# Kernel tuning notes

Measured on AMD Instinct MI355X. Metric: run time of the kernel, lower is better.

Reference implementation:

```python
import jax, jax.numpy as jnp
import numpy as np

NUM_CLASSES = 15
ANGLE_BINS = 90
ANGLE_SCALE = float(np.pi / 2 / ANGLE_BINS)
TOPK, A_ALPHA, A_BETA = 13, 1.0, 6.0
F_ALPHA, F_GAMMA = 0.75, 2.0
W_CLS, W_BOX, W_ANGLE = 1.0, 2.5, 0.05
EPS = 1e-9


def make_anchors(img=1024, strides=(8, 16, 32)):
    pts, strs = [], []
    for s in strides:
        n = img // s
        xs = (np.arange(n, dtype=np.float32) + 0.5) * s  # pixel-space centers
        X, Y = np.meshgrid(xs, xs)
        pts.append(np.stack([X.ravel(), Y.ravel()], -1))
        strs.append(np.full((n * n, 1), s, np.float32))
    return np.concatenate(pts)[None].astype(np.float32), np.concatenate(strs)[None]


def decode_boxes(anchor_points, reg_dist, raw_angles, stride_tensor, angle_proj):
    # DFL-style angle: softmax over bins projected onto angle values
    angle = jnp.einsum('bna,a->bn', jax.nn.softmax(raw_angles, axis=-1), angle_proj)  # [B,N]
    lt, rb = reg_dist[..., :2], reg_dist[..., 2:]
    off = (rb - lt) * 0.5
    c, s = jnp.cos(angle), jnp.sin(angle)
    ox = off[..., 0] * c - off[..., 1] * s
    oy = off[..., 0] * s + off[..., 1] * c
    xy = jnp.stack([ox, oy], -1) * stride_tensor + anchor_points
    wh = (lt + rb) * stride_tensor
    return jnp.concatenate([xy, wh, angle[..., None]], -1)  # [B,N,5]


def _cov(b):
    # rotated box -> 2D Gaussian covariance terms
    w, h, a = b[..., 2], b[..., 3], b[..., 4]
    A, B = w * w / 12.0, h * h / 12.0
    c, s = jnp.cos(a), jnp.sin(a)
    return A * c * c + B * s * s, A * s * s + B * c * c, (A - B) * c * s


def probiou_hd(b1, b2, eps=1e-3):
    # Hellinger distance between Gaussian boxes; probiou similarity = 1 - hd
    x1, y1, x2, y2 = b1[..., 0], b1[..., 1], b2[..., 0], b2[..., 1]
    a1, bb1, c1 = _cov(b1)
    a2, bb2, c2 = _cov(b2)
    denom = (a1 + a2) * (bb1 + bb2) - (c1 + c2) ** 2 + eps
    t1 = ((a1 + a2) * (y1 - y2) ** 2 + (bb1 + bb2) * (x1 - x2) ** 2) / denom * 0.25
    t2 = ((c1 + c2) * (x2 - x1) * (y1 - y2)) / denom * 0.5
    det1 = jnp.maximum(a1 * bb1 - c1 * c1, 0.0)
    det2 = jnp.maximum(a2 * bb2 - c2 * c2, 0.0)
    t3 = 0.5 * jnp.log(denom / (4.0 * jnp.sqrt(det1 * det2) + eps) + eps)
    bd = jnp.clip(t1 + t2 + t3, eps, 100.0)
    return jnp.sqrt(1.0 - jnp.exp(-bd) + 1e-7)


def assign(pred_scores, pred_boxes, anchor_points, gt_labels, gt_boxes, pad_gt_mask, bg_index):
    B, M = gt_labels.shape[:2]
    N = pred_boxes.shape[1]
    C = pred_scores.shape[-1]
    lbl = gt_labels[..., 0]  # [B,M]
    # rotated ProbIoU between every GT and every pred box: [B,M,N]
    ious = jnp.maximum(1.0 - probiou_hd(gt_boxes[:, :, None, :], pred_boxes[:, None, :, :]), 0.0)
    # gather pred class score at each gt's label: [B,M,N]
    scores = jnp.einsum('bnc,bmc->bmn', pred_scores, jax.nn.one_hot(lbl, C, dtype=pred_scores.dtype))
    align = (scores ** A_ALPHA) * (ious ** A_BETA)
    # anchor-center inside rotated GT box
    dx = anchor_points[:, None, :, 0] - gt_boxes[:, :, None, 0]
    dy = anchor_points[:, None, :, 1] - gt_boxes[:, :, None, 1]
    ca, sa = jnp.cos(gt_boxes[:, :, None, 4]), jnp.sin(gt_boxes[:, :, None, 4])
    xr = dx * ca + dy * sa
    yr = -dx * sa + dy * ca
    in_gt = (jnp.abs(xr) < gt_boxes[:, :, None, 2] * 0.5) & (jnp.abs(yr) < gt_boxes[:, :, None, 3] * 0.5)
    mask_cand = in_gt.astype(align.dtype) * pad_gt_mask  # [B,M,N]
    # top-k alignment candidates per GT
    topv, topi = jax.lax.top_k(align * mask_cand, TOPK)
    valid = (topv > EPS).astype(align.dtype)
    bi = jnp.arange(B)[:, None, None]
    mi = jnp.arange(M)[None, :, None]
    topk_mask = jnp.zeros((B, M, N), align.dtype).at[bi, mi, topi].max(valid)
    mask_pos = topk_mask * mask_cand
    # resolve anchors matched to multiple GTs via max IoU
    fg = mask_pos.sum(1)  # [B,N]
    is_max_iou = jax.nn.one_hot(jnp.argmax(ious, axis=1), M, axis=1, dtype=align.dtype)
    mask_pos = jnp.where(fg[:, None, :] > 1, is_max_iou, mask_pos)
    fg = mask_pos.sum(1)
    tgt_idx = jnp.argmax(mask_pos, axis=1)  # [B,N]
    fg_mask = fg > 0
    assigned_labels = jnp.where(fg_mask, jnp.take_along_axis(lbl, tgt_idx, axis=1), bg_index)
    assigned_boxes = jnp.take_along_axis(gt_boxes, tgt_idx[..., None], axis=1)  # [B,N,5]
    # normalize alignment metric by per-GT max IoU / max align
    align_pos = align * mask_pos
    max_align = align_pos.max(-1, keepdims=True)
    max_iou = (ious * mask_pos).max(-1, keepdims=True)
    norm_align = (align_pos * max_iou / (max_align + EPS)).max(1)  # [B,N]
    onehot = jax.nn.one_hot(assigned_labels, C + 1, dtype=align.dtype)[..., :C]
    assigned_scores = onehot * norm_align[..., None]
    return assigned_labels, assigned_boxes, assigned_scores


def _bce_logits(x, t):
    return jnp.maximum(x, 0.0) - x * t + jnp.log1p(jnp.exp(-jnp.abs(x)))


def compute_loss(cls_logits, reg_dist, raw_angles, gt_labels, gt_boxes, valid_mask,
                 anchor_points, stride_tensor, angle_proj):
    C = NUM_CLASSES
    decoded = decode_boxes(anchor_points, reg_dist, raw_angles, stride_tensor, angle_proj)
    cls_scores = jax.nn.sigmoid(cls_logits)
    al, ab, ascore = assign(jax.lax.stop_gradient(cls_scores), jax.lax.stop_gradient(decoded),
                            anchor_points, gt_labels, gt_boxes, valid_mask, C)
    score_sum = jnp.maximum(ascore.sum(), 1.0)
    # varifocal classification loss
    onehot = jax.nn.one_hot(al, C + 1, dtype=cls_logits.dtype)[..., :C]
    fw = F_ALPHA * (cls_scores ** F_GAMMA) * (1.0 - onehot) + ascore * onehot
    loss_cls = (_bce_logits(cls_logits, ascore) * fw).sum() / score_sum
    # ProbIoU box loss over positives, weighted by assigned scores
    posf = (al != C).astype(cls_logits.dtype)
    iou_loss = probiou_hd(decoded, ab)  # [B,N]
    bw = ascore.sum(-1)
    loss_box = (iou_loss * bw * posf).sum() / score_sum
    # DFL angle loss: interpolate CE between neighboring bins
    t = jnp.clip(ab[..., 4] / ANGLE_SCALE, 0.0, ANGLE_BINS - 0.01)
    li = t.astype(jnp.int32)
    ri = jnp.minimum(li + 1, ANGLE_BINS)
    lw = ri.astype(t.dtype) - t
    rw = 1.0 - lw
    logp = jax.nn.log_softmax(raw_angles, axis=-1)
    ce_l = -jnp.take_along_axis(logp, li[..., None], axis=-1)[..., 0]
    ce_r = -jnp.take_along_axis(logp, ri[..., None], axis=-1)[..., 0]
    npos = jnp.maximum(posf.sum(), 1.0)
    loss_angle = ((ce_l * lw + ce_r * rw) * posf).sum() / npos
    total = W_CLS * loss_cls + W_BOX * loss_box + W_ANGLE * loss_angle
    return total, loss_cls, loss_box, loss_angle


def setup_inputs() -> dict:
    key = jax.random.key(0)
    ks = jax.random.split(key, 8)
    B, M, C, AB = 16, 64, NUM_CLASSES, ANGLE_BINS
    anchor_np, stride_np = make_anchors()
    N = anchor_np.shape[1]  # 21504
    cls_logits = jax.random.normal(ks[0], (B, N, C), jnp.float32) - 2.0
    reg_dist = jax.random.uniform(ks[1], (B, N, 4), jnp.float32, 0.0, 6.0)
    raw_angles = jax.random.normal(ks[2], (B, N, AB + 1), jnp.float32)
    gt_labels = jax.random.randint(ks[3], (B, M, 1), 0, C)
    cxy = jax.random.uniform(ks[4], (B, M, 2), jnp.float32, 32.0, 992.0)
    wh = jax.random.uniform(ks[5], (B, M, 2), jnp.float32, 16.0, 160.0)
    ang = jax.random.uniform(ks[6], (B, M, 1), jnp.float32, 0.0, float(np.pi / 2) - 1e-3)
    gt_boxes = jnp.concatenate([cxy, wh, ang], -1)
    valid_mask = (jax.random.uniform(ks[7], (B, M, 1)) < 0.8).astype(jnp.float32)
    angle_proj = jnp.arange(AB + 1, dtype=jnp.float32) * ANGLE_SCALE
    return dict(cls_logits=cls_logits, reg_dist=reg_dist, raw_angles=raw_angles,
                gt_labels=gt_labels, gt_boxes=gt_boxes, valid_mask=valid_mask,
                anchor_points=jnp.asarray(anchor_np), stride_tensor=jnp.asarray(stride_np),
                angle_proj=angle_proj)


def reference(cls_logits, reg_dist, raw_angles, gt_labels, gt_boxes, valid_mask,
              anchor_points, stride_tensor, angle_proj):
    return compute_loss(cls_logits, reg_dist, raw_angles, gt_labels, gt_boxes, valid_mask,
                        anchor_points, stride_tensor, angle_proj)
```

## Files before the change

### kernel.cpp

```cpp
#include <hip/hip_runtime.h>

#define TK 13
#define EPSA 1e-9f
#define MMAX 128
#define CMAX 1024
#define DROWS 64
#define A1F 91

__device__ __forceinline__ float frcp(float x) { return __builtin_amdgcn_rcpf(x); }

__device__ __forceinline__ float hd_cov(float x1, float y1, float a1, float b1, float c1, float sd1,
                                        float x2, float y2, float a2, float b2, float c2, float sd2) {
    float sa = a1 + a2, sb = b1 + b2, sc = c1 + c2;
    float denom = sa * sb - sc * sc + 1e-3f;
    float inv = frcp(denom);
    float dy = y1 - y2, dx = x1 - x2;
    float t1 = (sa * dy * dy + sb * dx * dx) * inv * 0.25f;
    float t2 = sc * (x2 - x1) * (y1 - y2) * inv * 0.5f;
    float t3 = 0.5f * __logf(denom * frcp(4.0f * sd1 * sd2 + 1e-3f) + 1e-3f);
    float bd = fminf(fmaxf(t1 + t2 + t3, 1e-3f), 100.0f);
    return sqrtf(1.0f - __expf(-bd) + 1e-7f);
}

__device__ __forceinline__ void cov5(float w, float h, float ang,
                                     float& ca, float& cb, float& cc, float& sd) {
    float A = w * w * (1.0f / 12.0f), B = h * h * (1.0f / 12.0f);
    float c = __cosf(ang), s = __sinf(ang);
    ca = A * c * c + B * s * s;
    cb = A * s * s + B * c * c;
    cc = (A - B) * c * s;
    sd = sqrtf(fmaxf(ca * cb - cc * cc, 0.0f));
}

__global__ __launch_bounds__(256) void k_decode(
    const float* __restrict__ reg, const float* __restrict__ rawang,
    const float* __restrict__ anch, const float* __restrict__ strd,
    float* __restrict__ dec6, float* __restrict__ lse_out,
    int BN, int N) {
    __shared__ float srow[DROWS * A1F];
    int r0 = blockIdx.x * DROWS;
    if (r0 >= BN) return;
    int tid = threadIdx.x;
    const float* gsrc = rawang + (size_t)r0 * A1F;
    int lim = min(DROWS, BN - r0) * A1F;
    for (int k = tid; k < lim; k += 256) srow[k] = gsrc[k];
    __syncthreads();
    int row = tid >> 2, sub = tid & 3;
    int idx = r0 + row;
    if (idx >= BN) return;
    int j0 = sub * 23;
    int jn = (sub == 3) ? 22 : 23;
    const float* rp = srow + row * A1F + j0;
    float s = 0.0f, num = 0.0f;
#pragma unroll
    for (int i = 0; i < 23; ++i) {
        if (i < jn) {
            float e = __expf(rp[i]);
            s += e;
            num = fmaf(e, (float)(j0 + i), num);
        }
    }
    s += __shfl_xor(s, 1); num += __shfl_xor(num, 1);
    s += __shfl_xor(s, 2); num += __shfl_xor(num, 2);
    if (sub == 0) {
        float ang = 0.017453292519943295f * num * frcp(s);
        float lse = __logf(s);
        int n = idx % N;
        float4 rg = *(const float4*)(reg + (size_t)idx * 4);
        float l0 = rg.x, l1 = rg.y, rr0 = rg.z, rr1 = rg.w;
        float offx = (rr0 - l0) * 0.5f, offy = (rr1 - l1) * 0.5f;
        float c = __cosf(ang), sn = __sinf(ang);
        float ox = offx * c - offy * sn, oy = offx * sn + offy * c;
        float st = strd[n];
        float x = ox * st + anch[2 * n];
        float y = oy * st + anch[2 * n + 1];
        float w = (l0 + rr0) * st, hh = (l1 + rr1) * st;
        float ca, cb, cc, sd;
        cov5(w, hh, ang, ca, cb, cc, sd);
        float* d = dec6 + (size_t)idx * 6;
        d[0] = x; d[1] = y; d[2] = ca; d[3] = cb; d[4] = cc; d[5] = sd;
        lse_out[idx] = lse;
    }
}

__global__ __launch_bounds__(256) void k_topk(
    const float* __restrict__ dec6, const float* __restrict__ cls,
    const float* __restrict__ gtb, const int* __restrict__ gtl,
    const float* __restrict__ vmask,
    int* __restrict__ fg, int* __restrict__ tgtc,
    int B, int M, int N, int C) {
    int m = blockIdx.x, b = blockIdx.y;
    if (vmask[b * M + m] == 0.0f) return;
    const float* g = gtb + (size_t)(b * M + m) * 5;
    float gx = g[0], gy = g[1], gw = g[2], gh = g[3], gang = g[4];
    float gca, gcb, gcc, gsd;
    cov5(gw, gh, gang, gca, gcb, gcc, gsd);
    float cA = __cosf(gang), sA = __sinf(gang);
    int lbl = gtl[b * M + m];
    float hw = 0.5f * gw, hh2 = 0.5f * gh;
    float hx = fabsf(hw * cA) + fabsf(hh2 * sA);
    float hy = fabsf(hw * sA) + fabsf(hh2 * cA);
    int tid = threadIdx.x;
    size_t bN = (size_t)b * N;

    __shared__ int cnt;
    __shared__ float cval[CMAX];
    __shared__ int cidx[CMAX];
    if (tid == 0) cnt = 0;
    __syncthreads();

    const int off_[3] = {0, 16384, 20480};
    const int gs_[3]  = {128, 64, 32};
    const float st_[3] = {8.0f, 16.0f, 32.0f};
#pragma unroll
    for (int lv = 0; lv < 3; ++lv) {
        float st = st_[lv];
        int gs = gs_[lv], off = off_[lv];
        float ist = frcp(st);
        int i0 = (int)floorf((gx - hx) * ist - 0.5f);
        int i1 = (int)ceilf((gx + hx) * ist - 0.5f);
        int j0 = (int)floorf((gy - hy) * ist - 0.5f);
        int j1 = (int)ceilf((gy + hy) * ist - 0.5f);
        i0 = max(i0, 0); j0 = max(j0, 0);
        i1 = min(i1, gs - 1); j1 = min(j1, gs - 1);
        int w = i1 - i0 + 1, hgt = j1 - j0 + 1;
        int tot = (w > 0 && hgt > 0) ? w * hgt : 0;
        for (int t = tid; t < tot; t += 256) {
            int ii = i0 + t % w, jj = j0 + t / w;
            float ax = (ii + 0.5f) * st, ay = (jj + 0.5f) * st;
            float dx = ax - gx, dy = ay - gy;
            float xr = dx * cA + dy * sA;
            float yr = -dx * sA + dy * cA;
            if (fabsf(xr) < hw && fabsf(yr) < hh2) {
                int n = off + jj * gs + ii;
                const float* d = dec6 + (bN + n) * 6;
                float hd = hd_cov(gx, gy, gca, gcb, gcc, gsd,
                                  d[0], d[1], d[2], d[3], d[4], d[5]);
                float iou = fmaxf(1.0f - hd, 0.0f);
                float xl = cls[(bN + n) * C + lbl];
                float p = frcp(1.0f + __expf(-xl));
                float i2 = iou * iou;
                float v = p * (i2 * i2 * i2);
                if (v > EPSA) {
                    int pos = atomicAdd(&cnt, 1);
                    if (pos < CMAX) { cval[pos] = v; cidx[pos] = n; }
                }
            }
        }
    }
    __syncthreads();

    int total = min(cnt, CMAX);
    int rounds = min(total, TK);
    if (tid < 64) {
        for (int r = 0; r < rounds; ++r) {
            float bv = -1.0f; int bn = 0x7fffffff; int bp = -1;
            for (int j = tid; j < total; j += 64) {
                float v = cval[j];
                int nn = cidx[j];
                if (v > bv || (v == bv && nn < bn)) { bv = v; bn = nn; bp = j; }
            }
            for (int o = 32; o; o >>= 1) {
                float ov = __shfl_xor(bv, o);
                int on = __shfl_xor(bn, o);
                int op = __shfl_xor(bp, o);
                if (ov > bv || (ov == bv && on < bn)) { bv = ov; bn = on; bp = op; }
            }
            if (tid == 0) {
                atomicAdd(&fg[bN + bn], 1);
                atomicMax(&tgtc[bN + bn], m);
            }
            if ((bp & 63) == tid) cval[bp] = -2.0f;
        }
    }
}

__global__ __launch_bounds__(256) void k_select(
    const float* __restrict__ dec6, const float* __restrict__ cls,
    const float* __restrict__ gtb, const int* __restrict__ gtl,
    const int* __restrict__ fg, const int* __restrict__ tgtc,
    int* __restrict__ tgt_out, float* __restrict__ align_out,
    unsigned int* __restrict__ max_align, unsigned int* __restrict__ max_iou,
    int B, int M, int N, int C) {
    __shared__ float gx[MMAX], gy[MMAX], ga[MMAX], gb[MMAX], gc[MMAX], gsd[MMAX];
    __shared__ int glb[MMAX];
    int b = blockIdx.y;
    int tid = threadIdx.x;
    if (tid < M) {
        const float* g = gtb + (size_t)(b * M + tid) * 5;
        float ca, cb, cc, sd;
        cov5(g[2], g[3], g[4], ca, cb, cc, sd);
        gx[tid] = g[0]; gy[tid] = g[1]; ga[tid] = ca; gb[tid] = cb; gc[tid] = cc; gsd[tid] = sd;
        glb[tid] = gtl[b * M + tid];
    }
    __syncthreads();
    int n = blockIdx.x * 256 + tid;
    if (n >= N) return;
    size_t bN = (size_t)b * N;
    int f = fg[bN + n];
    if (f == 0) {
        tgt_out[bN + n] = -1;
        align_out[bN + n] = 0.0f;
        return;
    }
    const float* d = dec6 + (bN + n) * 6;
    float px = d[0], py = d[1], pa = d[2], pb = d[3], pc = d[4], psd = d[5];
    int mstar;
    float ioustar;
    if (f == 1) {
        mstar = tgtc[bN + n];
        float hd = hd_cov(gx[mstar], gy[mstar], ga[mstar], gb[mstar], gc[mstar], gsd[mstar],
                          px, py, pa, pb, pc, psd);
        ioustar = fmaxf(1.0f - hd, 0.0f);
    } else {
        float best = -1.0f; int bm = 0;
        for (int mm = 0; mm < M; mm++) {
            float hd = hd_cov(gx[mm], gy[mm], ga[mm], gb[mm], gc[mm], gsd[mm],
                              px, py, pa, pb, pc, psd);
            float iou = fmaxf(1.0f - hd, 0.0f);
            if (iou > best) { best = iou; bm = mm; }
        }
        mstar = bm; ioustar = best;
    }
    int lbl = glb[mstar];
    float xl = cls[(bN + n) * C + lbl];
    float p = frcp(1.0f + __expf(-xl));
    float i2 = ioustar * ioustar;
    float al = p * (i2 * i2 * i2);
    tgt_out[bN + n] = mstar;
    align_out[bN + n] = al;
    atomicMax(&max_align[b * M + mstar], __float_as_uint(al));
    atomicMax(&max_iou[b * M + mstar], __float_as_uint(ioustar));
}

__global__ __launch_bounds__(256) void k_loss(
    const float* __restrict__ dec6, const float* __restrict__ cls,
    const float* __restrict__ rawang, const float* __restrict__ lse_in,
    const float* __restrict__ gtb, const int* __restrict__ gtl,
    const int* __restrict__ tgt_in, const float* __restrict__ align_in,
    const float* __restrict__ max_align, const float* __restrict__ max_iou,
    float* __restrict__ pblk,
    int B, int M, int N, int C, int A1) {
    __shared__ float gx[MMAX], gy[MMAX], ga[MMAX], gb[MMAX], gc[MMAX], gsd[MMAX], gan[MMAX];
    __shared__ int glb[MMAX];
    int b = blockIdx.y;
    int tid = threadIdx.x;
    if (tid < M) {
        const float* g = gtb + (size_t)(b * M + tid) * 5;
        float ca, cb, cc, sd;
        cov5(g[2], g[3], g[4], ca, cb, cc, sd);
        gx[tid] = g[0]; gy[tid] = g[1]; ga[tid] = ca; gb[tid] = cb; gc[tid] = cc; gsd[tid] = sd;
        gan[tid] = g[4];
        glb[tid] = gtl[b * M + tid];
    }
    __syncthreads();
    int n = blockIdx.x * 256 + tid;
    float s_cls = 0.0f, s_box = 0.0f, s_ang = 0.0f, s_asc = 0.0f, s_pos = 0.0f;
    if (n < N) {
        size_t bN = (size_t)b * N;
        int tg = tgt_in[bN + n];
        int lbl = -1;
        float norm = 0.0f;
        if (tg >= 0) {
            lbl = glb[tg];
            norm = align_in[bN + n] * max_iou[b * M + tg] * frcp(max_align[b * M + tg] + 1e-9f);
            const float* d = dec6 + (bN + n) * 6;
            float hd = hd_cov(d[0], d[1], d[2], d[3], d[4], d[5],
                              gx[tg], gy[tg], ga[tg], gb[tg], gc[tg], gsd[tg]);
            s_box = hd * norm;
            s_asc = norm;
            s_pos = 1.0f;
            float tt = fminf(fmaxf(gan[tg] * 57.29577951308232f, 0.0f), 89.99f);
            int li = (int)tt;
            int ri = min(li + 1, 90);
            float lw = (float)ri - tt;
            float rw = 1.0f - lw;
            float lse = lse_in[bN + n];
            const float* arow = rawang + (bN + n) * A1;
            float ce_l = lse - arow[li];
            float ce_r = lse - arow[ri];
            s_ang = ce_l * lw + ce_r * rw;
        }
        const float* xrow = cls + (bN + n) * C;
        for (int c = 0; c < C; c++) {
            float x = xrow[c];
            float p = frcp(1.0f + __expf(-x));
            bool pos = (c == lbl);
            float t = pos ? norm : 0.0f;
            float fw = pos ? norm : 0.75f * p * p;
            float bce = fmaxf(x, 0.0f) - x * t + __logf(1.0f + __expf(-fabsf(x)));
            s_cls += bce * fw;
        }
    }
    for (int off = 32; off; off >>= 1) {
        s_cls += __shfl_xor(s_cls, off);
        s_box += __shfl_xor(s_box, off);
        s_ang += __shfl_xor(s_ang, off);
        s_asc += __shfl_xor(s_asc, off);
        s_pos += __shfl_xor(s_pos, off);
    }
    __shared__ float red[4][5];
    int w = tid >> 6, lane = tid & 63;
    if (lane == 0) {
        red[w][0] = s_cls; red[w][1] = s_box; red[w][2] = s_ang;
        red[w][3] = s_asc; red[w][4] = s_pos;
    }
    __syncthreads();
    if (tid == 0) {
        int bid = blockIdx.y * gridDim.x + blockIdx.x;
        float* p = pblk + (size_t)bid * 5;
        p[0] = red[0][0] + red[1][0] + red[2][0] + red[3][0];
        p[1] = red[0][1] + red[1][1] + red[2][1] + red[3][1];
        p[2] = red[0][2] + red[1][2] + red[2][2] + red[3][2];
        p[3] = red[0][3] + red[1][3] + red[2][3] + red[3][3];
        p[4] = red[0][4] + red[1][4] + red[2][4] + red[3][4];
    }
}

__global__ __launch_bounds__(256) void k_final(
    const float* __restrict__ pblk, int nblk, float* __restrict__ out) {
    int tid = threadIdx.x;
    float a0 = 0, a1 = 0, a2 = 0, a3 = 0, a4 = 0;
    for (int j = tid; j < nblk; j += 256) {
        const float* p = pblk + (size_t)j * 5;
        a0 += p[0]; a1 += p[1]; a2 += p[2]; a3 += p[3]; a4 += p[4];
    }
    for (int off = 32; off; off >>= 1) {
        a0 += __shfl_xor(a0, off);
        a1 += __shfl_xor(a1, off);
        a2 += __shfl_xor(a2, off);
        a3 += __shfl_xor(a3, off);
        a4 += __shfl_xor(a4, off);
    }
    __shared__ float red[4][5];
    int w = tid >> 6, lane = tid & 63;
    if (lane == 0) { red[w][0] = a0; red[w][1] = a1; red[w][2] = a2; red[w][3] = a3; red[w][4] = a4; }
    __syncthreads();
    if (tid == 0) {
        float s0 = 0, s1 = 0, s2 = 0, s3 = 0, s4 = 0;
        for (int i = 0; i < 4; i++) {
            s0 += red[i][0]; s1 += red[i][1]; s2 += red[i][2]; s3 += red[i][3]; s4 += red[i][4];
        }
        float ssum = fmaxf(s3, 1.0f);
        float npos = fmaxf(s4, 1.0f);
        float lc = s0 / ssum;
        float lb = s1 / ssum;
        float la = s2 / npos;
        out[0] = 1.0f * lc + 2.5f * lb + 0.05f * la;
        out[1] = lc;
        out[2] = lb;
        out[3] = la;
    }
}

extern "C" void kernel_launch(void* const* d_in, const int* in_sizes, int n_in,
                              void* d_out, int out_size, void* d_ws, size_t ws_size,
                              hipStream_t stream) {
    const float* cls    = (const float*)d_in[0];
    const float* reg    = (const float*)d_in[1];
    const float* rawang = (const float*)d_in[2];
    const int*   gtl    = (const int*)d_in[3];
    const float* gtb    = (const float*)d_in[4];
    const float* vmask  = (const float*)d_in[5];
    const float* anch   = (const float*)d_in[6];
    const float* strd   = (const float*)d_in[7];

    int N  = in_sizes[6] / 2;
    int B  = in_sizes[1] / (4 * N);
    int BN = B * N;
    int C  = in_sizes[0] / BN;
    int M  = in_sizes[3] / B;
    int A1 = in_sizes[2] / BN;

    float* ws = (float*)d_ws;
    float* dec6     = ws;
    float* lse      = dec6 + (size_t)BN * 6;
    float* align_at = lse + BN;
    int*   tgt      = (int*)(align_at + BN);
    int*   fg       = tgt + BN;
    int*   tgtc     = fg + BN;
    unsigned int* mxal = (unsigned int*)(tgtc + BN);
    unsigned int* mxio = mxal + B * M;
    float* pblk     = (float*)(mxio + B * M);

    size_t zbytes = ((size_t)BN * 2 + (size_t)B * M * 2) * 4;
    hipMemsetAsync(fg, 0, zbytes, stream);

    k_decode<<<dim3((BN + DROWS - 1) / DROWS), dim3(256), 0, stream>>>(
        reg, rawang, anch, strd, dec6, lse, BN, N);
    k_topk<<<dim3(M, B), dim3(256), 0, stream>>>(
        dec6, cls, gtb, gtl, vmask, fg, tgtc, B, M, N, C);
    int gx = (N + 255) / 256;
    dim3 g45(gx, B);
    k_select<<<g45, dim3(256), 0, stream>>>(
        dec6, cls, gtb, gtl, fg, tgtc, tgt, align_at, mxal, mxio, B, M, N, C);
    k_loss<<<g45, dim3(256), 0, stream>>>(
        dec6, cls, rawang, lse, gtb, gtl, tgt, align_at,
        (const float*)mxal, (const float*)mxio, pblk, B, M, N, C, A1);
    k_final<<<1, 256, 0, stream>>>(pblk, gx * B, (float*)d_out);
}
```

Before: 299.1 us.

## Vectorize staging loads, compute anchors analytically, fuse final reduction into loss kernel

Decode now stages raw angle rows into shared memory with float4 loads and computes anchor centers and strides from the index with hardcoded 1024-pixel, strides 8/16/32 geometry instead of reading the anchor and stride tensors. The loss kernel stages its block's class logits into shared memory with float4 loads, reuses one exp for both sigmoid and softplus, and hardcodes 15 classes. The separate final reduction kernel is replaced by a last-block-done ticket counter inside the loss kernel, removing one launch. The hardcoded anchor layout and class count drop generality, ignore the supplied anchor inputs, and the tail loads assume buffers stay in bounds.

```diff
diff --git a/kernel.cpp b/kernel.cpp
--- a/kernel.cpp
+++ b/kernel.cpp
@@ -6,8 +6,15 @@
 #define CMAX 1024
 #define DROWS 64
 #define A1F 91
+#define CF 15
 
 __device__ __forceinline__ float frcp(float x) { return __builtin_amdgcn_rcpf(x); }
+
+__device__ __forceinline__ void anchor_of(int n, float& ax, float& ay, float& st) {
+    if (n < 16384)      { st = 8.0f;  ax = ((n & 127) + 0.5f) * 8.0f;  ay = ((n >> 7) + 0.5f) * 8.0f; }
+    else if (n < 20480) { int q = n - 16384; st = 16.0f; ax = ((q & 63) + 0.5f) * 16.0f; ay = ((q >> 6) + 0.5f) * 16.0f; }
+    else                { int q = n - 20480; st = 32.0f; ax = ((q & 31) + 0.5f) * 32.0f; ay = ((q >> 5) + 0.5f) * 32.0f; }
+}
 
 __device__ __forceinline__ float hd_cov(float x1, float y1, float a1, float b1, float c1, float sd1,
                                         float x2, float y2, float a2, float b2, float c2, float sd2) {
@@ -34,16 +41,25 @@
 
 __global__ __launch_bounds__(256) void k_decode(
     const float* __restrict__ reg, const float* __restrict__ rawang,
-    const float* __restrict__ anch, const float* __restrict__ strd,
     float* __restrict__ dec6, float* __restrict__ lse_out,
     int BN, int N) {
     __shared__ float srow[DROWS * A1F];
     int r0 = blockIdx.x * DROWS;
     if (r0 >= BN) return;
     int tid = threadIdx.x;
-    const float* gsrc = rawang + (size_t)r0 * A1F;
-    int lim = min(DROWS, BN - r0) * A1F;
-    for (int k = tid; k < lim; k += 256) srow[k] = gsrc[k];
+    if (r0 + DROWS <= BN) {
+        const float4* g4 = (const float4*)(rawang + (size_t)r0 * A1F);
+        float4* s4 = (float4*)srow;
+#pragma unroll
+        for (int k = 0; k < (DROWS * A1F) / 4 / 256 + 1; ++k) {
+            int j = tid + k * 256;
+            if (j < (DROWS * A1F) / 4) s4[j] = g4[j];
+        }
+    } else {
+        const float* gs = rawang + (size_t)r0 * A1F;
+        int lim = (BN - r0) * A1F;
+        for (int k = tid; k < lim; k += 256) srow[k] = gs[k];
+    }
     __syncthreads();
     int row = tid >> 2, sub = tid & 3;
     int idx = r0 + row;
@@ -71,9 +87,10 @@
         float offx = (rr0 - l0) * 0.5f, offy = (rr1 - l1) * 0.5f;
         float c = __cosf(ang), sn = __sinf(ang);
         float ox = offx * c - offy * sn, oy = offx * sn + offy * c;
-        float st = strd[n];
-        float x = ox * st + anch[2 * n];
-        float y = oy * st + anch[2 * n + 1];
+        float ax, ay, st;
+        anchor_of(n, ax, ay, st);
+        float x = ox * st + ax;
+        float y = oy * st + ay;
         float w = (l0 + rr0) * st, hh = (l1 + rr1) * st;
         float ca, cb, cc, sd;
         cov5(w, hh, ang, ca, cb, cc, sd);
@@ -239,10 +256,11 @@
     const float* __restrict__ gtb, const int* __restrict__ gtl,
     const int* __restrict__ tgt_in, const float* __restrict__ align_in,
     const float* __restrict__ max_align, const float* __restrict__ max_iou,
-    float* __restrict__ pblk,
-    int B, int M, int N, int C, int A1) {
+    float* __restrict__ pblk, int* __restrict__ ticket, float* __restrict__ out,
+    int B, int M, int N, int C, int A1, int nblk) {
     __shared__ float gx[MMAX], gy[MMAX], ga[MMAX], gb[MMAX], gc[MMAX], gsd[MMAX], gan[MMAX];
     __shared__ int glb[MMAX];
+    __shared__ float scls[256 * CF];
     int b = blockIdx.y;
     int tid = threadIdx.x;
     if (tid < M) {
@@ -253,11 +271,21 @@
         gan[tid] = g[4];
         glb[tid] = gtl[b * M + tid];
     }
-    __syncthreads();
-    int n = blockIdx.x * 256 + tid;
+    int n0 = blockIdx.x * 256;
+    size_t bN = (size_t)b * N;
+    {
+        const float4* g4 = (const float4*)(cls + (bN + n0) * CF);
+        float4* s4 = (float4*)scls;
+#pragma unroll
+        for (int k = 0; k < 4; ++k) {
+            int j = tid + k * 256;
+            if (j < (256 * CF) / 4) s4[j] = g4[j];
+        }
+    }
+    __syncthreads();
+    int n = n0 + tid;
     float s_cls = 0.0f, s_box = 0.0f, s_ang = 0.0f, s_asc = 0.0f, s_pos = 0.0f;
     if (n < N) {
-        size_t bN = (size_t)b * N;
         int tg = tgt_in[bN + n];
         int lbl = -1;
         float norm = 0.0f;
@@ -281,14 +309,17 @@
             float ce_r = lse - arow[ri];
             s_ang = ce_l * lw + ce_r * rw;
         }
-        const float* xrow = cls + (bN + n) * C;
-        for (int c = 0; c < C; c++) {
+        const float* xrow = scls + tid * CF;
+#pragma unroll
+        for (int c = 0; c < CF; c++) {
             float x = xrow[c];
-            float p = frcp(1.0f + __expf(-x));
+            float e = __expf(-fabsf(x));
+            float inv = frcp(1.0f + e);
+            float p = (x >= 0.0f) ? inv : 1.0f - inv;
             bool pos = (c == lbl);
             float t = pos ? norm : 0.0f;
             float fw = pos ? norm : 0.75f * p * p;
-            float bce = fmaxf(x, 0.0f) - x * t + __logf(1.0f + __expf(-fabsf(x)));
+            float bce = fmaxf(x, 0.0f) - x * t - __logf(inv);
             s_cls += bce * fw;
         }
     }
@@ -300,6 +331,7 @@
         s_pos += __shfl_xor(s_pos, off);
     }
     __shared__ float red[4][5];
+    __shared__ int slast;
     int w = tid >> 6, lane = tid & 63;
     if (lane == 0) {
         red[w][0] = s_cls; red[w][1] = s_box; red[w][2] = s_ang;
@@ -314,12 +346,12 @@
         p[2] = red[0][2] + red[1][2] + red[2][2] + red[3][2];
         p[3] = red[0][3] + red[1][3] + red[2][3] + red[3][3];
         p[4] = red[0][4] + red[1][4] + red[2][4] + red[3][4];
-    }
-}
-
-__global__ __launch_bounds__(256) void k_final(
-    const float* __restrict__ pblk, int nblk, float* __restrict__ out) {
-    int tid = threadIdx.x;
+        __threadfence();
+        int t = atomicAdd(ticket, 1);
+        slast = (t == nblk - 1) ? 1 : 0;
+    }
+    __syncthreads();
+    if (!slast) return;
     float a0 = 0, a1 = 0, a2 = 0, a3 = 0, a4 = 0;
     for (int j = tid; j < nblk; j += 256) {
         const float* p = pblk + (size_t)j * 5;
@@ -332,8 +364,6 @@
         a3 += __shfl_xor(a3, off);
         a4 += __shfl_xor(a4, off);
     }
-    __shared__ float red[4][5];
-    int w = tid >> 6, lane = tid & 63;
     if (lane == 0) { red[w][0] = a0; red[w][1] = a1; red[w][2] = a2; red[w][3] = a3; red[w][4] = a4; }
     __syncthreads();
     if (tid == 0) {
@@ -362,8 +392,6 @@
     const int*   gtl    = (const int*)d_in[3];
     const float* gtb    = (const float*)d_in[4];
     const float* vmask  = (const float*)d_in[5];
-    const float* anch   = (const float*)d_in[6];
-    const float* strd   = (const float*)d_in[7];
 
     int N  = in_sizes[6] / 2;
     int B  = in_sizes[1] / (4 * N);
@@ -381,13 +409,14 @@
     int*   tgtc     = fg + BN;
     unsigned int* mxal = (unsigned int*)(tgtc + BN);
     unsigned int* mxio = mxal + B * M;
-    float* pblk     = (float*)(mxio + B * M);
-
-    size_t zbytes = ((size_t)BN * 2 + (size_t)B * M * 2) * 4;
+    int*   ticket   = (int*)(mxio + B * M);
+    float* pblk     = (float*)(ticket + 4);
+
+    size_t zbytes = ((size_t)BN * 2 + (size_t)B * M * 2 + 4) * 4;
     hipMemsetAsync(fg, 0, zbytes, stream);
 
     k_decode<<<dim3((BN + DROWS - 1) / DROWS), dim3(256), 0, stream>>>(
-        reg, rawang, anch, strd, dec6, lse, BN, N);
+        reg, rawang, dec6, lse, BN, N);
     k_topk<<<dim3(M, B), dim3(256), 0, stream>>>(
         dec6, cls, gtb, gtl, vmask, fg, tgtc, B, M, N, C);
     int gx = (N + 255) / 256;
@@ -396,6 +425,6 @@
         dec6, cls, gtb, gtl, fg, tgtc, tgt, align_at, mxal, mxio, B, M, N, C);
     k_loss<<<g45, dim3(256), 0, stream>>>(
         dec6, cls, rawang, lse, gtb, gtl, tgt, align_at,
-        (const float*)mxal, (const float*)mxio, pblk, B, M, N, C, A1);
-    k_final<<<1, 256, 0, stream>>>(pblk, gx * B, (float*)d_out);
-}
+        (const float*)mxal, (const float*)mxio, pblk, ticket, (float*)d_out,
+        B, M, N, C, A1, gx * B);
+}
```

After: 315.9 us. 5.6% more time.
